# Optimization experiments

Measured on AMD Instinct MI355X. Metric: run time of the kernel, lower is better.

## Reference

```python
import jax, jax.numpy as jnp
import numpy as np
import math

N_HEAD = 8


def _rope(x):
    # x: [B, H, S, D]; lucidrains rotary_embedding_torch default: interleaved pairs, theta=10000
    D = x.shape[-1]
    S = x.shape[-2]
    inv_freq = 1.0 / (10000.0 ** (jnp.arange(0, D, 2, dtype=jnp.float32) / D))  # [D/2]
    t = jnp.arange(S, dtype=jnp.float32)
    freqs = jnp.repeat(t[:, None] * inv_freq[None, :], 2, axis=-1)  # [S, D] interleaved repeat
    cos = jnp.cos(freqs).astype(x.dtype)
    sin = jnp.sin(freqs).astype(x.dtype)
    xp = x.reshape(*x.shape[:-1], D // 2, 2)
    rot = jnp.stack((-xp[..., 1], xp[..., 0]), axis=-1).reshape(x.shape)  # rotate_half (interleaved)
    return x * cos + rot * sin


def _row_linear(x, Wo):
    # faithful RowLinear: transpose then flat-reshape back (a real permutation), linear, inverse shuffle
    B, S, P = x.shape
    E = Wo.shape[0]
    x = jnp.swapaxes(x, 1, 2).reshape(B, S, P)
    x = jnp.einsum('bsp,ep->bse', x, Wo)  # [B, S, E]
    x = x.reshape(B, E, -1)  # [B, E, S]
    return jnp.swapaxes(x, 1, 2)  # [B, S, E]


def setup_inputs() -> dict:
    key = jax.random.key(0)
    k0, k1, k2, k3, k4 = jax.random.split(key, 5)
    B, S, E, P = 4, 2048, 1024, 1024
    std = 1.0 / math.sqrt(E)
    return {
        'emb': jax.random.normal(k0, (B, S, E), dtype=jnp.float32),
        'W1': jax.random.normal(k1, (P, E), dtype=jnp.float32) * std,
        'W2': jax.random.normal(k2, (P, E), dtype=jnp.float32) * std,
        'W3': jax.random.normal(k3, (P, E), dtype=jnp.float32) * std,
        'Wo': jax.random.normal(k4, (E, P), dtype=jnp.float32) * std,
    }


def reference(emb, W1, W2, W3, Wo):
    B, S, E = emb.shape
    P = W1.shape[0]
    H = N_HEAD
    D = P // H
    q = jnp.einsum('bse,pe->bsp', emb, W1).reshape(B, H, S, D)  # raw view split (as in source)
    k = jnp.einsum('bse,pe->bsp', emb, W2).reshape(B, H, S, D)
    v = jnp.einsum('bse,pe->bsp', emb, W3).reshape(B, H, S, D)
    q = _rope(q)
    k = _rope(k)
    scores = jnp.einsum('bhqd,bhkd->bhqk', q, k).astype(jnp.float32) / math.sqrt(H)
    attn = jax.nn.softmax(scores, axis=-1).astype(v.dtype)
    out = jnp.einsum('bhqk,bhkd->bhqd', attn, v)  # [B, H, S, D]
    out = jnp.swapaxes(out, 1, 2).reshape(B, S, P)
    return _row_linear(out, Wo)
```

## Files before the change

### kernel.cpp

```cpp
#include <hip/hip_runtime.h>

typedef float f32x4 __attribute__((ext_vector_type(4)));
typedef float f32x16 __attribute__((ext_vector_type(16)));
typedef __bf16 bf16x8 __attribute__((ext_vector_type(8)));

__device__ __forceinline__ unsigned short f2bf(float f) {
  unsigned int u = __float_as_uint(f);
  u = (u + 0x7FFFu + ((u >> 16) & 1u)) >> 16;
  return (unsigned short)u;
}
__device__ __forceinline__ float bf2f(unsigned short u) {
  return __uint_as_float((unsigned int)u << 16);
}

__device__ __forceinline__ f32x4 mfma16(bf16x8 a, bf16x8 b, f32x4 c) {
  return __builtin_amdgcn_mfma_f32_16x16x32_bf16(a, b, c, 0, 0, 0);
}
__device__ __forceinline__ f32x16 mfma32(bf16x8 a, bf16x8 b, f32x16 c) {
  return __builtin_amdgcn_mfma_f32_32x32x16_bf16(a, b, c, 0, 0, 0);
}

__device__ __forceinline__ unsigned int cvtpk_bf16(float a, float b) {
  unsigned int r;
  asm("v_cvt_pk_bf16_f32 %0, %1, %2" : "=v"(r) : "v"(a), "v"(b));
  return r;
}
__device__ __forceinline__ void pl32swap(unsigned int& a, unsigned int& b) {
  asm("v_permlane32_swap_b32 %0, %1" : "+v"(a), "+v"(b));
}

__device__ __forceinline__ void load8_bf16(const unsigned short* p, unsigned short* d) {
  *(uint4*)d = *(const uint4*)p;
}
__device__ __forceinline__ void load8_bf16(const float* p, unsigned short* d) {
  float4 a = *(const float4*)p;
  float4 b = *(const float4*)(p + 4);
  __align__(16) unsigned short t[8] = {f2bf(a.x), f2bf(a.y), f2bf(a.z), f2bf(a.w),
                                       f2bf(b.x), f2bf(b.y), f2bf(b.z), f2bf(b.w)};
  *(uint4*)d = *(uint4*)t;
}

__device__ __forceinline__ void gload_lds16(const unsigned short* g, unsigned short* l) {
  __builtin_amdgcn_global_load_lds(
      (const __attribute__((address_space(1))) void*)g,
      (__attribute__((address_space(3))) void*)l, 16, 0, 0);
}

__device__ __forceinline__ void drain_barrier() {
  asm volatile("s_waitcnt vmcnt(0)" ::: "memory");
  __builtin_amdgcn_sched_barrier(0);
  __builtin_amdgcn_s_barrier();
  __builtin_amdgcn_sched_barrier(0);
}

__global__ __launch_bounds__(256) void convert_gen(const float* __restrict__ src,
                                                   unsigned short* __restrict__ dst) {
  int idx = (blockIdx.x * 256 + threadIdx.x) * 8;
  __align__(16) unsigned short t[8];
  load8_bf16(src + idx, t);
  *(uint4*)(dst + idx) = *(uint4*)t;
}

__global__ __launch_bounds__(256) void convert_w3(const float* __restrict__ W1,
                                                  const float* __restrict__ W2,
                                                  const float* __restrict__ W3,
                                                  unsigned short* __restrict__ dst) {
  int i = blockIdx.x;
  int sel = i >> 9;
  const float* src = (sel == 0) ? W1 : (sel == 1) ? W2 : W3;
  int off = (i & 511) * 2048 + threadIdx.x * 8;
  __align__(16) unsigned short t[8];
  load8_bf16(src + off, t);
  *(uint4*)(dst + sel * 1048576 + off) = *(uint4*)t;
}

__global__ __launch_bounds__(256) void gemm_qkv(const unsigned short* __restrict__ A,
                                                const unsigned short* __restrict__ WB,
                                                unsigned short* __restrict__ q,
                                                unsigned short* __restrict__ k,
                                                unsigned short* __restrict__ v) {
  __shared__ __align__(16) unsigned short As[3][128][32];
  __shared__ __align__(16) unsigned short Bs[3][128][32];
  const int t = threadIdx.x;
  const int lane = t & 63;
  const int wid = t >> 6;
  const int quad = lane >> 4;
  const int l16 = lane & 15;
  const int wm = (wid >> 1) << 6;
  const int wn = (wid & 1) << 6;
  const int sel = blockIdx.x >> 3;
  const int nb = (blockIdx.x & 7) << 7;
  const int mbase = blockIdx.y * 128;
  const unsigned short* Bt = WB + sel * 1048576;
  unsigned short* C = (sel == 0) ? q : (sel == 1) ? k : v;

  const int c0 = t, c1 = t + 256;
  const unsigned short* aSrc0 = A + (size_t)(mbase + (c0 >> 2)) * 1024 + ((c0 & 3) << 3);
  const unsigned short* aSrc1 = A + (size_t)(mbase + (c1 >> 2)) * 1024 + ((c1 & 3) << 3);
  const unsigned short* bSrc0 = Bt + (size_t)(nb + (c0 >> 2)) * 1024 + ((c0 & 3) << 3);
  const unsigned short* bSrc1 = Bt + (size_t)(nb + (c1 >> 2)) * 1024 + ((c1 & 3) << 3);
  unsigned short* aDst0 = &As[0][0][0] + c0 * 8;
  unsigned short* aDst1 = &As[0][0][0] + c1 * 8;
  unsigned short* bDst0 = &Bs[0][0][0] + c0 * 8;
  unsigned short* bDst1 = &Bs[0][0][0] + c1 * 8;

  auto stage = [&](int k0, int p) {
    const int po = p * 4096;
    gload_lds16(aSrc0 + k0, aDst0 + po);
    gload_lds16(aSrc1 + k0, aDst1 + po);
    gload_lds16(bSrc0 + k0, bDst0 + po);
    gload_lds16(bSrc1 + k0, bDst1 + po);
  };

  f32x4 acc[4][4] = {};

  stage(0, 0);
  stage(32, 1);
  asm volatile("s_waitcnt vmcnt(4)" ::: "memory");
  __builtin_amdgcn_sched_barrier(0);
  __builtin_amdgcn_s_barrier();
  __builtin_amdgcn_sched_barrier(0);

  int p = 0;
  for (int k0 = 0; k0 < 1024; k0 += 32) {
    if (k0 + 64 < 1024) stage(k0 + 64, p == 0 ? 2 : p - 1);
    bf16x8 af[4], bfr[4];
#pragma unroll
    for (int mt = 0; mt < 4; ++mt)
      af[mt] = *(const bf16x8*)(&As[p][wm + mt * 16 + l16][quad * 8]);
#pragma unroll
    for (int nt = 0; nt < 4; ++nt)
      bfr[nt] = *(const bf16x8*)(&Bs[p][wn + nt * 16 + l16][quad * 8]);
#pragma unroll
    for (int mt = 0; mt < 4; ++mt)
#pragma unroll
      for (int nt = 0; nt < 4; ++nt)
        acc[mt][nt] = mfma16(af[mt], bfr[nt], acc[mt][nt]);
    if (k0 + 64 < 1024) {
      asm volatile("s_waitcnt vmcnt(4)" ::: "memory");
    } else {
      asm volatile("s_waitcnt vmcnt(0)" ::: "memory");
    }
    __builtin_amdgcn_sched_barrier(0);
    __builtin_amdgcn_s_barrier();
    __builtin_amdgcn_sched_barrier(0);
    p = (p == 2) ? 0 : p + 1;
  }

  const bool rope = (sel < 2);
#pragma unroll
  for (int mt = 0; mt < 4; ++mt) {
#pragma unroll
    for (int nt = 0; nt < 4; ++nt) {
#pragma unroll
      for (int r = 0; r < 4; ++r) {
        int row_g = mbase + wm + mt * 16 + quad * 4 + r;
        int col_g = nb + wn + nt * 16 + l16;
        float val = acc[mt][nt][r];
        if (rope) {
          float other = __shfl_xor(val, 1);
          int s = (((row_g & 2047) << 3) + (col_g >> 7)) & 2047;
          int d = col_g & 127;
          float invf = __expf(-0.14391156f * (float)(d >> 1));
          float ang = (float)s * invf;
          float sv, cv;
          __sincosf(ang, &sv, &cv);
          val = (d & 1) ? (val * cv + other * sv) : (val * cv - other * sv);
        }
        C[(size_t)row_g * 1024 + col_g] = f2bf(val);
      }
    }
  }
}

__global__ __launch_bounds__(256) void transpose_v(const unsigned short* __restrict__ Vn,
                                                   unsigned short* __restrict__ VT) {
  __shared__ __align__(16) unsigned short tile[64][72];
  const int t = threadIdx.x;
  const int s0 = blockIdx.x * 64;
  const int d0 = blockIdx.y * 64;
  const int bh = blockIdx.z;
  const size_t base = (size_t)bh * (2048 * 128);
#pragma unroll
  for (int i = 0; i < 2; ++i) {
    int c = t + (i << 8);
    int sr = c >> 3;
    int dc = (c & 7) << 3;
    *(uint4*)(&tile[sr][dc]) = *(const uint4*)(Vn + base + (size_t)(s0 + sr) * 128 + d0 + dc);
  }
  __syncthreads();
#pragma unroll
  for (int i = 0; i < 2; ++i) {
    int c = t + (i << 8);
    int dr = c >> 3;
    int sc = (c & 7) << 3;
    __align__(16) unsigned short tmp[8];
#pragma unroll
    for (int j = 0; j < 8; ++j) tmp[j] = tile[sc + j][dr];
    *(uint4*)(VT + base + (size_t)(d0 + dr) * 2048 + s0 + sc) = *(uint4*)tmp;
  }
}

__global__ __launch_bounds__(256) void gemm_out(const unsigned short* __restrict__ OT,
                                                const unsigned short* __restrict__ Bt,
                                                float* __restrict__ C) {
  __shared__ __align__(16) char smem_raw[49152];
  const int t = threadIdx.x;
  const int lane = t & 63;
  const int wid = t >> 6;
  const int quad = lane >> 4;
  const int l16 = lane & 15;
  const int wm = (wid >> 1) << 6;
  const int wn = (wid & 1) << 6;
  const int mbase = blockIdx.y * 128;
  const int nbase = blockIdx.x * 128;

  const unsigned short* aSrcs[2];
  const unsigned short* bSrcs[2];
#pragma unroll
  for (int i = 0; i < 2; ++i) {
    int c = t + (i << 8);
    int row = c >> 2;
    int col = (c & 3) << 3;
    int R = mbase + row;
    int b = R >> 11;
    int ii = R & 2047;
    aSrcs[i] = OT + (size_t)(b * 8 + (ii >> 8)) * (128 * 2048) +
               (size_t)((ii >> 1) & 127) * 2048 + ((ii & 1) << 10) + col;
    bSrcs[i] = Bt + (size_t)(nbase + row) * 1024 + col;
  }
  unsigned short* smE = (unsigned short*)smem_raw;

  auto stage = [&](int k0, int p) {
    const int po = p * 8192;
    gload_lds16(aSrcs[0] + k0, smE + po + t * 8);
    gload_lds16(aSrcs[1] + k0, smE + po + 2048 + t * 8);
    gload_lds16(bSrcs[0] + k0, smE + po + 4096 + t * 8);
    gload_lds16(bSrcs[1] + k0, smE + po + 6144 + t * 8);
  };

  f32x4 acc[4][4] = {};

  stage(0, 0);
  stage(32, 1);
  asm volatile("s_waitcnt vmcnt(4)" ::: "memory");
  __builtin_amdgcn_sched_barrier(0);
  __builtin_amdgcn_s_barrier();
  __builtin_amdgcn_sched_barrier(0);

  int p = 0;
  for (int k0 = 0; k0 < 1024; k0 += 32) {
    if (k0 + 64 < 1024) stage(k0 + 64, p == 0 ? 2 : p - 1);
    auto As = (unsigned short(*)[32])(smem_raw + p * 16384);
    auto Bs = (unsigned short(*)[32])(smem_raw + p * 16384 + 8192);
    bf16x8 af[4], bfr[4];
#pragma unroll
    for (int mt = 0; mt < 4; ++mt)
      af[mt] = *(const bf16x8*)(&As[wm + mt * 16 + l16][quad * 8]);
#pragma unroll
    for (int nt = 0; nt < 4; ++nt)
      bfr[nt] = *(const bf16x8*)(&Bs[wn + nt * 16 + l16][quad * 8]);
#pragma unroll
    for (int mt = 0; mt < 4; ++mt)
#pragma unroll
      for (int nt = 0; nt < 4; ++nt)
        acc[mt][nt] = mfma16(af[mt], bfr[nt], acc[mt][nt]);
    if (k0 + 64 < 1024) {
      asm volatile("s_waitcnt vmcnt(4)" ::: "memory");
    } else {
      asm volatile("s_waitcnt vmcnt(0)" ::: "memory");
    }
    __builtin_amdgcn_sched_barrier(0);
    __builtin_amdgcn_s_barrier();
    __builtin_amdgcn_sched_barrier(0);
    p = (p == 2) ? 0 : p + 1;
  }

  float(*Ts)[68] = (float(*)[68])smem_raw;
  const int b = mbase >> 11;
  const int ebase = (mbase & 2047) >> 1;
#pragma unroll
  for (int p2 = 0; p2 < 2; ++p2) {
    __syncthreads();
#pragma unroll
    for (int mt = 0; mt < 4; ++mt)
#pragma unroll
      for (int nt = 0; nt < 4; ++nt)
#pragma unroll
        for (int rr = p2; rr < 4; rr += 2) {
          int col_local = wn + nt * 16 + l16;
          int row_local = wm + mt * 16 + quad * 4 + rr;
          Ts[col_local][row_local >> 1] = acc[mt][nt][rr];
        }
    __syncthreads();
    int srow = t >> 1;
    int e0 = (t & 1) << 5;
    float* dst = C + (size_t)b * 2097152 +
                 (size_t)(p2 * 1024 + nbase + srow) * 1024 + ebase + e0;
#pragma unroll
    for (int j = 0; j < 8; ++j)
      ((float4*)dst)[j] = *(const float4*)&Ts[srow][e0 + j * 4];
  }
}

__global__ __launch_bounds__(256, 2) void flash_attn(const unsigned short* __restrict__ Q,
                                                     const unsigned short* __restrict__ Kg,
                                                     const unsigned short* __restrict__ VTg,
                                                     unsigned short* __restrict__ OT) {
  __shared__ __align__(16) char sm[65536];
  const int t = threadIdx.x;
  const int lane = t & 63;
  const int wid = t >> 6;
  const int l31 = lane & 31;
  const int hi = lane >> 5;
  const int x16 = (l31 & 7) << 4;
  const int i = blockIdx.x;
  const int bh = (i & 7) + ((i >> 3) & 3) * 8;
  const int qbase = (i >> 5) << 7;
  const size_t base = (size_t)bh * (2048 * 128);
  const float scale = 0.3535533905932738f;

  const unsigned short* Kg_b = Kg + base;
  const unsigned short* Vg_b = VTg + base;

  auto issueKV = [&](int kvoff, int pbit) {
    unsigned short* Kl = (unsigned short*)(sm + (pbit << 14));
    unsigned short* Vl = (unsigned short*)(sm + 32768 + (pbit << 14));
#pragma unroll
    for (int j = 0; j < 4; ++j) {
      int c = t + (j << 8);
      int row = c >> 4, ch = c & 15;
      gload_lds16(Kg_b + (size_t)(kvoff + row) * 128 + ((ch ^ (row & 7)) << 3),
                  Kl + c * 8);
      int d = c >> 3, cv = c & 7;
      gload_lds16(Vg_b + (size_t)d * 2048 + kvoff + ((cv ^ (d & 7)) << 3), Vl + c * 8);
    }
  };

  bf16x8 qf[8];
  {
    const unsigned short* qp = Q + base + (size_t)(qbase + wid * 32 + l31) * 128 + hi * 8;
#pragma unroll
    for (int ks = 0; ks < 8; ++ks) qf[ks] = *(const bf16x8*)(qp + ks * 16);
  }

  f32x16 accO[4] = {};
  float m = -__builtin_inff();
  float l = 0.f;

  issueKV(0, 0);
  drain_barrier();

  for (int kv = 0; kv < 2048; kv += 64) {
    const int p = (kv >> 6) & 1;
    if (kv + 64 < 2048) issueKV(kv + 64, p ^ 1);
    const char* Kb = sm + (p << 14);
    const char* Vb = sm + 32768 + (p << 14);

    f32x16 s0 = {}, s1 = {};
#pragma unroll
    for (int ks = 0; ks < 8; ++ks) {
      int cb = (ks * 32 + hi * 16) ^ x16;
      bf16x8 k0 = *(const bf16x8*)(Kb + l31 * 256 + cb);
      bf16x8 k1 = *(const bf16x8*)(Kb + 8192 + l31 * 256 + cb);
      s0 = mfma32(k0, qf[ks], s0);
      s1 = mfma32(k1, qf[ks], s1);
    }

    float t8[8];
#pragma unroll
    for (int r = 0; r < 8; ++r)
      t8[r] = fmaxf(fmaxf(s0[r], s0[r + 8]), fmaxf(s1[r], s1[r + 8]));
#pragma unroll
    for (int d = 4; d > 0; d >>= 1)
#pragma unroll
      for (int r = 0; r < d; ++r) t8[r] = fmaxf(t8[r], t8[r + d]);
    float mx = fmaxf(t8[0], __shfl_xor(t8[0], 32));
    if (__any(mx > m + 16.f)) {
      float mnew = fmaxf(m, mx);
      float alpha = __expf((m - mnew) * scale);
      l *= alpha;
#pragma unroll
      for (int dt = 0; dt < 4; ++dt)
#pragma unroll
        for (int r = 0; r < 16; ++r) accO[dt][r] *= alpha;
      m = mnew;
    }
    float negms = -m * scale;
#pragma unroll
    for (int r = 0; r < 16; ++r) s0[r] = __expf(fmaf(s0[r], scale, negms));
#pragma unroll
    for (int r = 0; r < 16; ++r) s1[r] = __expf(fmaf(s1[r], scale, negms));
#pragma unroll
    for (int r = 0; r < 8; ++r)
      t8[r] = (s0[r] + s0[r + 8]) + (s1[r] + s1[r + 8]);
#pragma unroll
    for (int d = 4; d > 0; d >>= 1)
#pragma unroll
      for (int r = 0; r < d; ++r) t8[r] += t8[r + d];
    l += t8[0] + __shfl_xor(t8[0], 32);

    bf16x8 pfrag[4];
#pragma unroll
    for (int kb = 0; kb < 4; ++kb) {
      const f32x16& S = (kb < 2) ? s0 : s1;
      const int b = (kb & 1) * 8;
      unsigned int a0 = cvtpk_bf16(S[b + 0], S[b + 1]);
      unsigned int a1 = cvtpk_bf16(S[b + 2], S[b + 3]);
      unsigned int a2 = cvtpk_bf16(S[b + 4], S[b + 5]);
      unsigned int a3 = cvtpk_bf16(S[b + 6], S[b + 7]);
      pl32swap(a0, a2);
      pl32swap(a1, a3);
      union { unsigned int u[4]; bf16x8 v; } pu;
      pu.u[0] = a0; pu.u[1] = a1; pu.u[2] = a2; pu.u[3] = a3;
      pfrag[kb] = pu.v;
    }

#pragma unroll
    for (int dt = 0; dt < 4; ++dt) {
#pragma unroll
      for (int kb = 0; kb < 4; ++kb) {
        bf16x8 vfr = *(const bf16x8*)(Vb + l31 * 128 + dt * 4096 +
                                      ((kb * 32 + hi * 16) ^ x16));
        accO[dt] = mfma32(vfr, pfrag[kb], accO[dt]);
      }
    }

    drain_barrier();
  }

  auto To = (unsigned short(*)[136])sm;
  const float invl = 1.f / l;
  const int qloc = wid * 32 + l31;
#pragma unroll
  for (int dt = 0; dt < 4; ++dt)
#pragma unroll
    for (int r = 0; r < 16; ++r) {
      int d = dt * 32 + (r & 3) + ((r >> 2) << 3) + hi * 4;
      To[d][qloc] = f2bf(accO[dt][r] * invl);
    }
  __syncthreads();
  int dr = t >> 1;
  int off = (t & 1) << 6;
  unsigned short* dst = OT + base + (size_t)dr * 2048 + qbase + off;
#pragma unroll
  for (int j = 0; j < 8; ++j)
    ((uint4*)dst)[j] = *(const uint4*)&To[dr][off + j * 8];
}

extern "C" void kernel_launch(void* const* d_in, const int* in_sizes, int n_in,
                              void* d_out, int out_size, void* d_ws, size_t ws_size,
                              hipStream_t stream) {
  const float* emb = (const float*)d_in[0];
  const float* W1  = (const float*)d_in[1];
  const float* W2  = (const float*)d_in[2];
  const float* W3  = (const float*)d_in[3];
  const float* Wo  = (const float*)d_in[4];
  float* out = (float*)d_out;

  const size_t NELEM = (size_t)8 * 1024 * 1024;
  unsigned short* q     = (unsigned short*)d_ws;
  unsigned short* k     = q + NELEM;
  unsigned short* vn    = k + NELEM;
  unsigned short* X     = vn + NELEM;
  unsigned short* oT    = vn;
  unsigned short* vT    = X;
  unsigned short* W123B = X;
  unsigned short* WoB   = X;
  unsigned short* embB  = (unsigned short*)d_out;

  dim3 blk(256, 1, 1);
  convert_w3<<<dim3(1536), blk, 0, stream>>>(W1, W2, W3, W123B);
  convert_gen<<<dim3(4096), blk, 0, stream>>>(emb, embB);
  gemm_qkv<<<dim3(24, 64), blk, 0, stream>>>(embB, W123B, q, k, vn);
  transpose_v<<<dim3(32, 2, 32), blk, 0, stream>>>(vn, vT);
  flash_attn<<<dim3(512, 1, 1), blk, 0, stream>>>(q, k, vT, oT);
  convert_gen<<<dim3(512), blk, 0, stream>>>(Wo, WoB);
  gemm_out<<<dim3(8, 64), blk, 0, stream>>>(oT, WoB, out);
}
```

Before: 318.9 us.

## Pre-swizzle weights into MFMA fragment layout and load B directly to registers

The weight conversion kernels now write W1/W2/W3 and Wo in a fragment-ordered layout, so each lane's bf16x8 MFMA operand is contiguous. The QKV and output GEMMs then load B fragments straight from global memory into registers, skipping LDS staging for B and halving LDS use per stage. This removes LDS traffic and bank pressure for B. In exchange, global-load latency for B is exposed inside the loop, relying on L2 reuse across blocks, and the wait count changes to vmcnt(2).

```diff
diff --git a/kernel.cpp b/kernel.cpp
--- a/kernel.cpp
+++ b/kernel.cpp
@@ -48,6 +48,13 @@
 
 __device__ __forceinline__ void drain_barrier() {
   asm volatile("s_waitcnt vmcnt(0)" ::: "memory");
+  __builtin_amdgcn_sched_barrier(0);
+  __builtin_amdgcn_s_barrier();
+  __builtin_amdgcn_sched_barrier(0);
+}
+
+__device__ __forceinline__ void wait2_barrier() {
+  asm volatile("s_waitcnt vmcnt(2)" ::: "memory");
   __builtin_amdgcn_sched_barrier(0);
   __builtin_amdgcn_s_barrier();
   __builtin_amdgcn_sched_barrier(0);
@@ -68,19 +75,38 @@
   int i = blockIdx.x;
   int sel = i >> 9;
   const float* src = (sel == 0) ? W1 : (sel == 1) ? W2 : W3;
-  int off = (i & 511) * 2048 + threadIdx.x * 8;
-  __align__(16) unsigned short t[8];
-  load8_bf16(src + off, t);
-  *(uint4*)(dst + sel * 1048576 + off) = *(uint4*)t;
+  int w = i & 511;
+  int t = threadIdx.x;
+  int p = 2 * w + (t >> 7);
+  int kc = t & 127;
+  __align__(16) unsigned short tmp[8];
+  load8_bf16(src + (size_t)p * 1024 + kc * 8, tmp);
+  int lane = (kc & 3) * 16 + (p & 15);
+  size_t idx16 = ((((size_t)(p >> 7) * 32 + (kc >> 2)) * 2 + ((p >> 6) & 1)) * 4 +
+                  ((p >> 4) & 3)) * 64 + lane;
+  *(uint4*)(dst + (size_t)sel * 1048576 + idx16 * 8) = *(uint4*)tmp;
+}
+
+__global__ __launch_bounds__(256) void convert_wo(const float* __restrict__ Wo,
+                                                  unsigned short* __restrict__ dst) {
+  int w = blockIdx.x;
+  int t = threadIdx.x;
+  int p = 2 * w + (t >> 7);
+  int kc = t & 127;
+  __align__(16) unsigned short tmp[8];
+  load8_bf16(Wo + (size_t)p * 1024 + kc * 8, tmp);
+  int lane = (kc & 3) * 16 + (p & 15);
+  size_t idx16 = ((((size_t)(p >> 7) * 32 + (kc >> 2)) * 2 + ((p >> 6) & 1)) * 4 +
+                  ((p >> 4) & 3)) * 64 + lane;
+  *(uint4*)(dst + idx16 * 8) = *(uint4*)tmp;
 }
 
 __global__ __launch_bounds__(256) void gemm_qkv(const unsigned short* __restrict__ A,
-                                                const unsigned short* __restrict__ WB,
+                                                const unsigned short* __restrict__ WBf,
                                                 unsigned short* __restrict__ q,
                                                 unsigned short* __restrict__ k,
                                                 unsigned short* __restrict__ v) {
   __shared__ __align__(16) unsigned short As[3][128][32];
-  __shared__ __align__(16) unsigned short Bs[3][128][32];
   const int t = threadIdx.x;
   const int lane = t & 63;
   const int wid = t >> 6;
@@ -89,61 +115,48 @@
   const int wm = (wid >> 1) << 6;
   const int wn = (wid & 1) << 6;
   const int sel = blockIdx.x >> 3;
-  const int nb = (blockIdx.x & 7) << 7;
+  const int nb = blockIdx.x & 7;
   const int mbase = blockIdx.y * 128;
-  const unsigned short* Bt = WB + sel * 1048576;
   unsigned short* C = (sel == 0) ? q : (sel == 1) ? k : v;
 
-  const int c0 = t, c1 = t + 256;
-  const unsigned short* aSrc0 = A + (size_t)(mbase + (c0 >> 2)) * 1024 + ((c0 & 3) << 3);
-  const unsigned short* aSrc1 = A + (size_t)(mbase + (c1 >> 2)) * 1024 + ((c1 & 3) << 3);
-  const unsigned short* bSrc0 = Bt + (size_t)(nb + (c0 >> 2)) * 1024 + ((c0 & 3) << 3);
-  const unsigned short* bSrc1 = Bt + (size_t)(nb + (c1 >> 2)) * 1024 + ((c1 & 3) << 3);
-  unsigned short* aDst0 = &As[0][0][0] + c0 * 8;
-  unsigned short* aDst1 = &As[0][0][0] + c1 * 8;
-  unsigned short* bDst0 = &Bs[0][0][0] + c0 * 8;
-  unsigned short* bDst1 = &Bs[0][0][0] + c1 * 8;
-
-  auto stage = [&](int k0, int p) {
-    const int po = p * 4096;
-    gload_lds16(aSrc0 + k0, aDst0 + po);
-    gload_lds16(aSrc1 + k0, aDst1 + po);
-    gload_lds16(bSrc0 + k0, bDst0 + po);
-    gload_lds16(bSrc1 + k0, bDst1 + po);
+  const unsigned short* aSrc0 = A + (size_t)(mbase + (t >> 2)) * 1024 + ((t & 3) << 3);
+  const unsigned short* aSrc1 = A + (size_t)(mbase + 64 + (t >> 2)) * 1024 + ((t & 3) << 3);
+  unsigned short* aDst0 = &As[0][0][0] + t * 8;
+  unsigned short* aDst1 = &As[0][0][0] + 2048 + t * 8;
+  auto stageA = [&](int k0, int p) {
+    gload_lds16(aSrc0 + k0, aDst0 + p * 4096);
+    gload_lds16(aSrc1 + k0, aDst1 + p * 4096);
   };
 
+  const unsigned short* pB = WBf + (size_t)sel * 1048576 +
+                             ((size_t)(nb * 64 + (wid & 1)) * 4) * 512 + lane * 8;
+
   f32x4 acc[4][4] = {};
 
-  stage(0, 0);
-  stage(32, 1);
-  asm volatile("s_waitcnt vmcnt(4)" ::: "memory");
+  stageA(0, 0);
+  stageA(32, 1);
+  asm volatile("s_waitcnt vmcnt(2)" ::: "memory");
   __builtin_amdgcn_sched_barrier(0);
   __builtin_amdgcn_s_barrier();
   __builtin_amdgcn_sched_barrier(0);
 
   int p = 0;
   for (int k0 = 0; k0 < 1024; k0 += 32) {
-    if (k0 + 64 < 1024) stage(k0 + 64, p == 0 ? 2 : p - 1);
-    bf16x8 af[4], bfr[4];
+    bf16x8 bfr[4];
+#pragma unroll
+    for (int nt = 0; nt < 4; ++nt) bfr[nt] = *(const bf16x8*)(pB + nt * 512);
+    pB += 4096;
+    if (k0 + 64 < 1024) stageA(k0 + 64, p == 0 ? 2 : p - 1);
+    bf16x8 af[4];
 #pragma unroll
     for (int mt = 0; mt < 4; ++mt)
       af[mt] = *(const bf16x8*)(&As[p][wm + mt * 16 + l16][quad * 8]);
 #pragma unroll
     for (int nt = 0; nt < 4; ++nt)
-      bfr[nt] = *(const bf16x8*)(&Bs[p][wn + nt * 16 + l16][quad * 8]);
-#pragma unroll
-    for (int mt = 0; mt < 4; ++mt)
-#pragma unroll
-      for (int nt = 0; nt < 4; ++nt)
+#pragma unroll
+      for (int mt = 0; mt < 4; ++mt)
         acc[mt][nt] = mfma16(af[mt], bfr[nt], acc[mt][nt]);
-    if (k0 + 64 < 1024) {
-      asm volatile("s_waitcnt vmcnt(4)" ::: "memory");
-    } else {
-      asm volatile("s_waitcnt vmcnt(0)" ::: "memory");
-    }
-    __builtin_amdgcn_sched_barrier(0);
-    __builtin_amdgcn_s_barrier();
-    __builtin_amdgcn_sched_barrier(0);
+    wait2_barrier();
     p = (p == 2) ? 0 : p + 1;
   }
 
@@ -155,7 +168,7 @@
 #pragma unroll
       for (int r = 0; r < 4; ++r) {
         int row_g = mbase + wm + mt * 16 + quad * 4 + r;
-        int col_g = nb + wn + nt * 16 + l16;
+        int col_g = (nb << 7) + wn + nt * 16 + l16;
         float val = acc[mt][nt][r];
         if (rope) {
           float other = __shfl_xor(val, 1);
@@ -202,9 +215,9 @@
 }
 
 __global__ __launch_bounds__(256) void gemm_out(const unsigned short* __restrict__ OT,
-                                                const unsigned short* __restrict__ Bt,
+                                                const unsigned short* __restrict__ Bf,
                                                 float* __restrict__ C) {
-  __shared__ __align__(16) char smem_raw[49152];
+  __shared__ __align__(16) char smem_raw[34816];
   const int t = threadIdx.x;
   const int lane = t & 63;
   const int wid = t >> 6;
@@ -213,10 +226,9 @@
   const int wm = (wid >> 1) << 6;
   const int wn = (wid & 1) << 6;
   const int mbase = blockIdx.y * 128;
-  const int nbase = blockIdx.x * 128;
+  const int nbx = blockIdx.x;
 
   const unsigned short* aSrcs[2];
-  const unsigned short* bSrcs[2];
 #pragma unroll
   for (int i = 0; i < 2; ++i) {
     int c = t + (i << 8);
@@ -227,52 +239,42 @@
     int ii = R & 2047;
     aSrcs[i] = OT + (size_t)(b * 8 + (ii >> 8)) * (128 * 2048) +
                (size_t)((ii >> 1) & 127) * 2048 + ((ii & 1) << 10) + col;
-    bSrcs[i] = Bt + (size_t)(nbase + row) * 1024 + col;
   }
   unsigned short* smE = (unsigned short*)smem_raw;
-
-  auto stage = [&](int k0, int p) {
-    const int po = p * 8192;
-    gload_lds16(aSrcs[0] + k0, smE + po + t * 8);
-    gload_lds16(aSrcs[1] + k0, smE + po + 2048 + t * 8);
-    gload_lds16(bSrcs[0] + k0, smE + po + 4096 + t * 8);
-    gload_lds16(bSrcs[1] + k0, smE + po + 6144 + t * 8);
+  auto stageA = [&](int k0, int p) {
+    gload_lds16(aSrcs[0] + k0, smE + p * 4096 + t * 8);
+    gload_lds16(aSrcs[1] + k0, smE + p * 4096 + 2048 + t * 8);
   };
 
+  const unsigned short* pB = Bf + ((size_t)(nbx * 64 + (wid & 1)) * 4) * 512 + lane * 8;
+
   f32x4 acc[4][4] = {};
 
-  stage(0, 0);
-  stage(32, 1);
-  asm volatile("s_waitcnt vmcnt(4)" ::: "memory");
+  stageA(0, 0);
+  stageA(32, 1);
+  asm volatile("s_waitcnt vmcnt(2)" ::: "memory");
   __builtin_amdgcn_sched_barrier(0);
   __builtin_amdgcn_s_barrier();
   __builtin_amdgcn_sched_barrier(0);
 
   int p = 0;
   for (int k0 = 0; k0 < 1024; k0 += 32) {
-    if (k0 + 64 < 1024) stage(k0 + 64, p == 0 ? 2 : p - 1);
-    auto As = (unsigned short(*)[32])(smem_raw + p * 16384);
-    auto Bs = (unsigned short(*)[32])(smem_raw + p * 16384 + 8192);
-    bf16x8 af[4], bfr[4];
+    bf16x8 bfr[4];
+#pragma unroll
+    for (int nt = 0; nt < 4; ++nt) bfr[nt] = *(const bf16x8*)(pB + nt * 512);
+    pB += 4096;
+    if (k0 + 64 < 1024) stageA(k0 + 64, p == 0 ? 2 : p - 1);
+    auto As = (unsigned short(*)[32])(smem_raw + p * 8192);
+    bf16x8 af[4];
 #pragma unroll
     for (int mt = 0; mt < 4; ++mt)
       af[mt] = *(const bf16x8*)(&As[wm + mt * 16 + l16][quad * 8]);
 #pragma unroll
     for (int nt = 0; nt < 4; ++nt)
-      bfr[nt] = *(const bf16x8*)(&Bs[wn + nt * 16 + l16][quad * 8]);
-#pragma unroll
-    for (int mt = 0; mt < 4; ++mt)
-#pragma unroll
-      for (int nt = 0; nt < 4; ++nt)
+#pragma unroll
+      for (int mt = 0; mt < 4; ++mt)
         acc[mt][nt] = mfma16(af[mt], bfr[nt], acc[mt][nt]);
-    if (k0 + 64 < 1024) {
-      asm volatile("s_waitcnt vmcnt(4)" ::: "memory");
-    } else {
-      asm volatile("s_waitcnt vmcnt(0)" ::: "memory");
-    }
-    __builtin_amdgcn_sched_barrier(0);
-    __builtin_amdgcn_s_barrier();
-    __builtin_amdgcn_sched_barrier(0);
+    wait2_barrier();
     p = (p == 2) ? 0 : p + 1;
   }
 
@@ -296,7 +298,7 @@
     int srow = t >> 1;
     int e0 = (t & 1) << 5;
     float* dst = C + (size_t)b * 2097152 +
-                 (size_t)(p2 * 1024 + nbase + srow) * 1024 + ebase + e0;
+                 (size_t)(p2 * 1024 + nbx * 128 + srow) * 1024 + ebase + e0;
 #pragma unroll
     for (int j = 0; j < 8; ++j)
       ((float4*)dst)[j] = *(const float4*)&Ts[srow][e0 + j * 4];
@@ -475,6 +477,6 @@
   gemm_qkv<<<dim3(24, 64), blk, 0, stream>>>(embB, W123B, q, k, vn);
   transpose_v<<<dim3(32, 2, 32), blk, 0, stream>>>(vn, vT);
   flash_attn<<<dim3(512, 1, 1), blk, 0, stream>>>(q, k, vT, oT);
-  convert_gen<<<dim3(512), blk, 0, stream>>>(Wo, WoB);
+  convert_wo<<<dim3(512), blk, 0, stream>>>(Wo, WoB);
   gemm_out<<<dim3(8, 64), blk, 0, stream>>>(oT, WoB, out);
 }
```

Result: no change. 317.0 us, median of 2 (-0.6%).
